# Kernel optimization log

Hardware: AMD Instinct MI355X
Metric: run time of the kernel (lower is better)

## Reference

```python
import jax, jax.numpy as jnp
import numpy as np

RESOLUTION = 128


def _bin_mask():
    # [4, 2] bool: corner i, dim d -> True if corner uses floor coord in dim d
    neigs = jnp.arange(4, dtype=jnp.int32)[:, None]
    dims = jnp.arange(2, dtype=jnp.int32)[None, :]
    return (neigs & (1 << dims)) == 0


def setup_inputs() -> dict:
    key = jax.random.key(0)
    k1, k2 = jax.random.split(key)
    batch = 65536
    res, map_num, feat_dim = RESOLUTION, 128, 8
    inputs = jax.random.uniform(k1, (batch, 2), dtype=jnp.float32)
    # xavier_uniform over [res^2, map_num*feat_dim]
    fan_in, fan_out = res * res, map_num * feat_dim
    bound = float(np.sqrt(6.0 / (fan_in + fan_out)))
    embeddings = jax.random.uniform(k2, (res * res, map_num * feat_dim),
                                    dtype=jnp.float32, minval=-bound, maxval=bound)
    return {"inputs": inputs, "embeddings": embeddings}


def reference(inputs, embeddings):
    res = RESOLUTION
    bin_mask = _bin_mask()                      # [4, 2]
    x = inputs * (res - 1)                      # [B, 2]
    xi = jnp.floor(x).astype(jnp.int32)         # [B, 2]
    xf = x - jax.lax.stop_gradient(jnp.floor(x))  # fractional part, grads flow via x
    xi = xi[:, None, :]                         # [B, 1, 2]
    xf = xf[:, None, :]                         # [B, 1, 2]
    neigs = jnp.where(bin_mask, xi, xi + 1)     # [B, 4, 2]
    ids = neigs[..., 0] * res + neigs[..., 1]   # [B, 4]
    neigs_features = embeddings[ids]            # [B, 4, D] irregular gather
    weights = jnp.where(bin_mask, 1.0 - xf, xf) # [B, 4, 2]
    w = jnp.prod(weights, axis=-1, keepdims=True)  # [B, 4, 1]
    return jnp.sum(neigs_features * w, axis=-2)    # [B, D]
```

## Files before the change

kernel.cpp:

```cpp
#include <hip/hip_runtime.h>

#define RES   128
#define FEAT  1024
#define NBINS (RES * RES)

typedef float nfloat4 __attribute__((ext_vector_type(4)));

__global__ __launch_bounds__(256)
void hist_kernel(const float* __restrict__ inputs, unsigned* __restrict__ hist, int N)
{
    int p = blockIdx.x * 256 + threadIdx.x;
    if (p >= N) return;
    const float2 uv = ((const float2*)inputs)[p];
    int i0 = (int)floorf(uv.x * (float)(RES - 1));
    int i1 = (int)floorf(uv.y * (float)(RES - 1));
    atomicAdd(&hist[i0 * RES + i1], 1u);
}

__global__ __launch_bounds__(256)
void scan_kernel(unsigned* __restrict__ hist)
{
    __shared__ unsigned part[256];
    int t = threadIdx.x;
    int base = t * 64;
    unsigned s = 0;
    for (int k = 0; k < 64; ++k) s += hist[base + k];
    part[t] = s;
    __syncthreads();
    if (t == 0) {
        unsigned run = 0;
        for (int i = 0; i < 256; ++i) { unsigned v = part[i]; part[i] = run; run += v; }
    }
    __syncthreads();
    unsigned run = part[t];
    for (int k = 0; k < 64; ++k) { unsigned v = hist[base + k]; hist[base + k] = run; run += v; }
}

__global__ __launch_bounds__(256)
void scatter_kernel(const float* __restrict__ inputs, unsigned* __restrict__ hist,
                    float4* __restrict__ sorted, int N)
{
    int p = blockIdx.x * 256 + threadIdx.x;
    if (p >= N) return;
    const float2 uv = ((const float2*)inputs)[p];
    int i0 = (int)floorf(uv.x * (float)(RES - 1));
    int i1 = (int)floorf(uv.y * (float)(RES - 1));
    unsigned pos = atomicAdd(&hist[i0 * RES + i1], 1u);
    float4 e;
    e.x = uv.x;
    e.y = uv.y;
    e.z = __uint_as_float((unsigned)p);
    e.w = 0.0f;
    sorted[pos] = e;
}

__global__ __launch_bounds__(256)
void DenseMap_cell_kernel(const float* __restrict__ emb,
                          const unsigned* __restrict__ hist,
                          const float4* __restrict__ sorted,
                          float* __restrict__ out,
                          int chunk)
{
    const int b    = blockIdx.x;
    const int cell = (b & 7) * chunk + (b >> 3);
    const int c    = threadIdx.x;

    const unsigned start = (cell == 0) ? 0u : hist[cell - 1];
    const unsigned end   = hist[cell];
    if (start == end) return;

    const int i0 = cell >> 7;
    const int i1 = cell & (RES - 1);

    const long base = (long)cell * FEAT;
    const float4 r00 = ((const float4*)(emb + base))[c];
    const float4 r01 = ((const float4*)(emb + base + FEAT))[c];
    const float4 r10 = ((const float4*)(emb + base + (long)RES * FEAT))[c];
    const float4 r11 = ((const float4*)(emb + base + (long)RES * FEAT + FEAT))[c];

    for (unsigned s = start; s < end; ++s) {
        const float4 e = sorted[s];
        const unsigned p = __float_as_uint(e.z);

        const float x0  = e.x * (float)(RES - 1);
        const float x1  = e.y * (float)(RES - 1);
        const float xf0 = x0 - (float)i0;
        const float xf1 = x1 - (float)i1;

        const float w00 = (1.0f - xf0) * (1.0f - xf1);
        const float w01 = (1.0f - xf0) * xf1;
        const float w10 = xf0 * (1.0f - xf1);
        const float w11 = xf0 * xf1;

        nfloat4 r;
        r.x = r00.x * w00 + r01.x * w01 + r10.x * w10 + r11.x * w11;
        r.y = r00.y * w00 + r01.y * w01 + r10.y * w10 + r11.y * w11;
        r.z = r00.z * w00 + r01.z * w01 + r10.z * w10 + r11.z * w11;
        r.w = r00.w * w00 + r01.w * w01 + r10.w * w10 + r11.w * w11;

        __builtin_nontemporal_store(r, ((nfloat4*)(out + (long)p * FEAT)) + c);
    }
}

__global__ __launch_bounds__(256)
void DenseMap_fallback_kernel(const float* __restrict__ inputs,
                              const float* __restrict__ emb,
                              float* __restrict__ out)
{
    const int p = blockIdx.x;
    const int c = threadIdx.x;

    const float x0 = inputs[2 * p + 0] * (float)(RES - 1);
    const float x1 = inputs[2 * p + 1] * (float)(RES - 1);
    const float f0 = floorf(x0);
    const float f1 = floorf(x1);
    const int   i0 = (int)f0;
    const int   i1 = (int)f1;
    const float xf0 = x0 - f0;
    const float xf1 = x1 - f1;

    const float w00 = (1.0f - xf0) * (1.0f - xf1);
    const float w01 = (1.0f - xf0) * xf1;
    const float w10 = xf0 * (1.0f - xf1);
    const float w11 = xf0 * xf1;

    const long base = (long)(i0 * RES + i1) * FEAT;
    const float4 a = ((const float4*)(emb + base))[c];
    const float4 b = ((const float4*)(emb + base + FEAT))[c];
    const float4 g = ((const float4*)(emb + base + (long)RES * FEAT))[c];
    const float4 h = ((const float4*)(emb + base + (long)RES * FEAT + FEAT))[c];

    float4 r;
    r.x = a.x * w00 + b.x * w01 + g.x * w10 + h.x * w11;
    r.y = a.y * w00 + b.y * w01 + g.y * w10 + h.y * w11;
    r.z = a.z * w00 + b.z * w01 + g.z * w10 + h.z * w11;
    r.w = a.w * w00 + b.w * w01 + g.w * w10 + h.w * w11;

    ((float4*)(out + (long)p * FEAT))[c] = r;
}

extern "C" void kernel_launch(void* const* d_in, const int* in_sizes, int n_in,
                              void* d_out, int out_size, void* d_ws, size_t ws_size,
                              hipStream_t stream)
{
    const float* inputs = (const float*)d_in[0];
    const float* emb    = (const float*)d_in[1];
    float*       out    = (float*)d_out;

    const int N = in_sizes[0] / 2;
    const size_t need = (size_t)N * sizeof(float4) + (size_t)NBINS * sizeof(unsigned);

    if (ws_size >= need) {
        float4*   sorted = (float4*)d_ws;
        unsigned* hist   = (unsigned*)(sorted + N);

        (void)hipMemsetAsync(hist, 0, NBINS * sizeof(unsigned), stream);
        hist_kernel<<<(N + 255) / 256, 256, 0, stream>>>(inputs, hist, N);
        scan_kernel<<<1, 256, 0, stream>>>(hist);
        scatter_kernel<<<(N + 255) / 256, 256, 0, stream>>>(inputs, hist, sorted, N);

        DenseMap_cell_kernel<<<NBINS, 256, 0, stream>>>(emb, hist, sorted, out, NBINS / 8);
    } else {
        DenseMap_fallback_kernel<<<N, 256, 0, stream>>>(inputs, emb, out);
    }
}
```

Baseline: 356.8 us.

## Fuse histogram, scan and scatter into one persistent kernel with grid barriers

```diff
diff --git a/kernel.cpp b/kernel.cpp
--- a/kernel.cpp
+++ b/kernel.cpp
@@ -6,52 +6,93 @@
 
 typedef float nfloat4 __attribute__((ext_vector_type(4)));
 
+__device__ inline void grid_barrier(unsigned* ctr, unsigned target)
+{
+    __syncthreads();
+    if (threadIdx.x == 0) {
+        __threadfence();
+        __hip_atomic_fetch_add(ctr, 1u, __ATOMIC_ACQ_REL, __HIP_MEMORY_SCOPE_AGENT);
+        while (__hip_atomic_load(ctr, __ATOMIC_ACQUIRE, __HIP_MEMORY_SCOPE_AGENT) < target) {
+            __builtin_amdgcn_s_sleep(2);
+        }
+        __threadfence();
+    }
+    __syncthreads();
+}
+
 __global__ __launch_bounds__(256)
-void hist_kernel(const float* __restrict__ inputs, unsigned* __restrict__ hist, int N)
-{
-    int p = blockIdx.x * 256 + threadIdx.x;
-    if (p >= N) return;
-    const float2 uv = ((const float2*)inputs)[p];
-    int i0 = (int)floorf(uv.x * (float)(RES - 1));
-    int i1 = (int)floorf(uv.y * (float)(RES - 1));
-    atomicAdd(&hist[i0 * RES + i1], 1u);
-}
-
-__global__ __launch_bounds__(256)
-void scan_kernel(unsigned* __restrict__ hist)
-{
-    __shared__ unsigned part[256];
-    int t = threadIdx.x;
-    int base = t * 64;
-    unsigned s = 0;
-    for (int k = 0; k < 64; ++k) s += hist[base + k];
-    part[t] = s;
-    __syncthreads();
-    if (t == 0) {
-        unsigned run = 0;
-        for (int i = 0; i < 256; ++i) { unsigned v = part[i]; part[i] = run; run += v; }
-    }
-    __syncthreads();
-    unsigned run = part[t];
-    for (int k = 0; k < 64; ++k) { unsigned v = hist[base + k]; hist[base + k] = run; run += v; }
-}
-
-__global__ __launch_bounds__(256)
-void scatter_kernel(const float* __restrict__ inputs, unsigned* __restrict__ hist,
-                    float4* __restrict__ sorted, int N)
-{
-    int p = blockIdx.x * 256 + threadIdx.x;
-    if (p >= N) return;
-    const float2 uv = ((const float2*)inputs)[p];
-    int i0 = (int)floorf(uv.x * (float)(RES - 1));
-    int i1 = (int)floorf(uv.y * (float)(RES - 1));
-    unsigned pos = atomicAdd(&hist[i0 * RES + i1], 1u);
-    float4 e;
-    e.x = uv.x;
-    e.y = uv.y;
-    e.z = __uint_as_float((unsigned)p);
-    e.w = 0.0f;
-    sorted[pos] = e;
+void sort_fused_kernel(const float* __restrict__ inputs,
+                       unsigned* __restrict__ hist,
+                       unsigned* __restrict__ bsum,
+                       unsigned* __restrict__ ctr,
+                       float4* __restrict__ sorted,
+                       int N)
+{
+    __shared__ unsigned sc[256];
+    const int t   = threadIdx.x;
+    const int tid = blockIdx.x * 256 + t;
+
+    float2 uv = make_float2(0.f, 0.f);
+    int cell = 0;
+    if (tid < N) {
+        uv = ((const float2*)inputs)[tid];
+        const int i0 = (int)floorf(uv.x * (float)(RES - 1));
+        const int i1 = (int)floorf(uv.y * (float)(RES - 1));
+        cell = i0 * RES + i1;
+        atomicAdd(&hist[cell], 1u);
+    }
+    grid_barrier(ctr, 256u);
+
+    if (blockIdx.x < 64) {
+        const int idx = blockIdx.x * 256 + t;
+        const unsigned v = __hip_atomic_load(&hist[idx], __ATOMIC_RELAXED,
+                                             __HIP_MEMORY_SCOPE_AGENT);
+        sc[t] = v;
+        __syncthreads();
+        for (int off = 1; off < 256; off <<= 1) {
+            const unsigned u = (t >= off) ? sc[t - off] : 0u;
+            __syncthreads();
+            sc[t] += u;
+            __syncthreads();
+        }
+        const unsigned incl = sc[t];
+        hist[idx] = incl - v;
+        if (t == 255)
+            __hip_atomic_store(&bsum[blockIdx.x], incl, __ATOMIC_RELAXED,
+                               __HIP_MEMORY_SCOPE_AGENT);
+    }
+    grid_barrier(ctr, 512u);
+
+    if (blockIdx.x == 0 && t < 64) {
+        unsigned v = __hip_atomic_load(&bsum[t], __ATOMIC_RELAXED,
+                                       __HIP_MEMORY_SCOPE_AGENT);
+        const unsigned orig = v;
+        for (int off = 1; off < 64; off <<= 1) {
+            const unsigned u = __shfl_up(v, off, 64);
+            if (t >= off) v += u;
+        }
+        __hip_atomic_store(&bsum[t], v - orig, __ATOMIC_RELAXED,
+                           __HIP_MEMORY_SCOPE_AGENT);
+    }
+    grid_barrier(ctr, 768u);
+
+    if (blockIdx.x < 64) {
+        const int idx = blockIdx.x * 256 + t;
+        const unsigned add = __hip_atomic_load(&bsum[blockIdx.x], __ATOMIC_RELAXED,
+                                               __HIP_MEMORY_SCOPE_AGENT);
+        hist[idx] += add;
+    }
+    grid_barrier(ctr, 1024u);
+
+    if (tid < N) {
+        const unsigned pos = atomicAdd(&hist[cell], 1u);
+        float4 e;
+        e.x = uv.x;
+        e.y = uv.y;
+        e.z = __uint_as_float((unsigned)tid);
+        e.w = 0.0f;
+        sorted[pos] = e;
+    }
 }
 
 __global__ __launch_bounds__(256)
@@ -78,27 +119,36 @@
     const float4 r10 = ((const float4*)(emb + base + (long)RES * FEAT))[c];
     const float4 r11 = ((const float4*)(emb + base + (long)RES * FEAT + FEAT))[c];
 
-    for (unsigned s = start; s < end; ++s) {
-        const float4 e = sorted[s];
-        const unsigned p = __float_as_uint(e.z);
-
-        const float x0  = e.x * (float)(RES - 1);
-        const float x1  = e.y * (float)(RES - 1);
-        const float xf0 = x0 - (float)i0;
-        const float xf1 = x1 - (float)i1;
-
-        const float w00 = (1.0f - xf0) * (1.0f - xf1);
-        const float w01 = (1.0f - xf0) * xf1;
-        const float w10 = xf0 * (1.0f - xf1);
-        const float w11 = xf0 * xf1;
-
-        nfloat4 r;
-        r.x = r00.x * w00 + r01.x * w01 + r10.x * w10 + r11.x * w11;
-        r.y = r00.y * w00 + r01.y * w01 + r10.y * w10 + r11.y * w11;
-        r.z = r00.z * w00 + r01.z * w01 + r10.z * w10 + r11.z * w11;
-        r.w = r00.w * w00 + r01.w * w01 + r10.w * w10 + r11.w * w11;
-
-        __builtin_nontemporal_store(r, ((nfloat4*)(out + (long)p * FEAT)) + c);
+    __shared__ float4 se[256];
+
+    for (unsigned cb = start; cb < end; cb += 256u) {
+        const int cnt = (int)min(end - cb, 256u);
+        if (c < cnt) se[c] = sorted[cb + c];
+        __syncthreads();
+
+        for (int j = 0; j < cnt; ++j) {
+            const float4 e = se[j];
+            const unsigned p = __float_as_uint(e.z);
+
+            const float x0  = e.x * (float)(RES - 1);
+            const float x1  = e.y * (float)(RES - 1);
+            const float xf0 = x0 - (float)i0;
+            const float xf1 = x1 - (float)i1;
+
+            const float w00 = (1.0f - xf0) * (1.0f - xf1);
+            const float w01 = (1.0f - xf0) * xf1;
+            const float w10 = xf0 * (1.0f - xf1);
+            const float w11 = xf0 * xf1;
+
+            nfloat4 r;
+            r.x = r00.x * w00 + r01.x * w01 + r10.x * w10 + r11.x * w11;
+            r.y = r00.y * w00 + r01.y * w01 + r10.y * w10 + r11.y * w11;
+            r.z = r00.z * w00 + r01.z * w01 + r10.z * w10 + r11.z * w11;
+            r.w = r00.w * w00 + r01.w * w01 + r10.w * w10 + r11.w * w11;
+
+            __builtin_nontemporal_store(r, ((nfloat4*)(out + (long)p * FEAT)) + c);
+        }
+        __syncthreads();
     }
 }
 
@@ -148,17 +198,17 @@
     float*       out    = (float*)d_out;
 
     const int N = in_sizes[0] / 2;
-    const size_t need = (size_t)N * sizeof(float4) + (size_t)NBINS * sizeof(unsigned);
-
-    if (ws_size >= need) {
+    const size_t aux  = (size_t)NBINS * sizeof(unsigned) + 256 * sizeof(unsigned);
+    const size_t need = (size_t)N * sizeof(float4) + aux;
+
+    if (N == 65536 && ws_size >= need) {
         float4*   sorted = (float4*)d_ws;
         unsigned* hist   = (unsigned*)(sorted + N);
-
-        (void)hipMemsetAsync(hist, 0, NBINS * sizeof(unsigned), stream);
-        hist_kernel<<<(N + 255) / 256, 256, 0, stream>>>(inputs, hist, N);
-        scan_kernel<<<1, 256, 0, stream>>>(hist);
-        scatter_kernel<<<(N + 255) / 256, 256, 0, stream>>>(inputs, hist, sorted, N);
-
+        unsigned* bsum   = hist + NBINS;
+        unsigned* ctr    = bsum + 64;
+
+        (void)hipMemsetAsync(hist, 0, aux, stream);
+        sort_fused_kernel<<<256, 256, 0, stream>>>(inputs, hist, bsum, ctr, sorted, N);
         DenseMap_cell_kernel<<<NBINS, 256, 0, stream>>>(emb, hist, sorted, out, NBINS / 8);
     } else {
         DenseMap_fallback_kernel<<<N, 256, 0, stream>>>(inputs, emb, out);
```

Measured after the change: 404.9 us. +13.5%, slower.
